# Kernel optimization log

Hardware: AMD Instinct MI355X
Metric: run time of the kernel (lower is better)

Reference implementation:

```python
import jax, jax.numpy as jnp
import numpy as np

B, N = 8192, 200  # batch of patches, fixed 200 points per patch


def setup_inputs() -> dict:
    key = jax.random.key(0)
    k1, = jax.random.split(key, 1)
    network_in = jax.random.normal(k1, (B, N, 13), dtype=jnp.float32)
    # learned parameters per build(): outward_shift init 0.25, a init 1, b init 0
    outward_shift = jnp.full((1,), 0.25, dtype=jnp.float32)
    a = jnp.ones((1,), dtype=jnp.float32)
    b = jnp.zeros((1,), dtype=jnp.float32)
    return {"network_in": network_in, "outward_shift": outward_shift, "a": a, "b": b}


def reference(network_in, outward_shift, a, b):
    w = network_in[:, :, 0:1]          # [B,N,1]
    xyz1 = network_in[:, :, 1:4]
    xyz2 = network_in[:, :, 4:7]       # also orig_xyz2
    norm1 = network_in[:, :, 7:10]
    norm2 = network_in[:, :, 10:13]

    w = jax.nn.relu(a * w + b) + 1e-8  # [B,N,1]

    v1 = xyz1 + norm1 * outward_shift
    v2 = xyz2 + norm2 * outward_shift

    w_sum = jnp.sum(w, axis=1)                       # [B,1]
    v1_ctr = jnp.sum(v1 * w, axis=1) / w_sum         # [B,3]
    v2_ctr = jnp.sum(v2 * w, axis=1) / w_sum         # [B,3]
    v1 = v1 - v1_ctr[:, None, :]
    v2 = v2 - v2_ctr[:, None, :]

    # cov = v2^T diag(w) v1, done without materializing the NxN diagonal
    cov = jnp.einsum('bni,bn,bnj->bij', v2, w[:, :, 0], v1)  # [B,3,3]

    # tf.linalg.svd: cov = u diag(s) v^T  ->  jnp svd: cov = u diag(s) vh, v = vh^T
    u, s, vh = jnp.linalg.svd(cov)
    v = jnp.swapaxes(vh, -1, -2)

    VUt = jnp.einsum('bik,bjk->bij', v, u)           # v @ u^T
    det_VUt = jnp.linalg.det(VUt)                    # [B]
    ones = jnp.ones_like(det_VUt)
    d = jnp.stack([ones, ones, det_VUt], axis=-1)    # [B,3]

    # R = v @ diag([1,1,det]) @ u^T
    R = jnp.einsum('bik,bk,bjk->bij', v, d, u)       # [B,3,3]

    t = v1_ctr - jnp.einsum('bij,bj->bi', R, v2_ctr) # [B,3]
    new_coords = jnp.einsum('bij,bnj->bni', R, xyz2) + t[:, None, :]
    return new_coords
```

## Files before the change

### kernel.cpp

```cpp
#include <hip/hip_runtime.h>
#include <math.h>

#define NPTS 200
#define NCH  13
#define BLK  256
#define FPB  (NPTS * NCH)

typedef float f4u __attribute__((ext_vector_type(4), aligned(4)));

__global__ __launch_bounds__(BLK) void reduce_kernel(
    const float* __restrict__ net_in,
    const float* __restrict__ shift_p,
    const float* __restrict__ a_p,
    const float* __restrict__ b_p,
    float* __restrict__ sums)
{
    __shared__ float s_in[4 * FPB];
    __shared__ float s_part[4][16][20];

    const int tid = threadIdx.x;
    const int w   = tid >> 6;
    const int l   = tid & 63;
    const int b   = blockIdx.x * 4 + w;

    const float shift = shift_p[0];
    const float aa    = a_p[0];
    const float bb    = b_p[0];

    const float* src = net_in + (size_t)b * FPB;
    float*       dst = s_in + w * FPB;

    #pragma unroll
    for (int j = 0; j < 10; ++j) {
        __builtin_amdgcn_global_load_lds(
            (const __attribute__((address_space(1))) void*)(src + j * 256 + l * 4),
            (__attribute__((address_space(3))) void*)(dst + j * 256),
            16, 0, 0);
    }
    if (l < 10) {
        __builtin_amdgcn_global_load_lds(
            (const __attribute__((address_space(1))) void*)(src + 2560 + l * 4),
            (__attribute__((address_space(3))) void*)(dst + 2560),
            16, 0, 0);
    }
    __builtin_amdgcn_s_waitcnt(0);
    __asm__ __volatile__("" ::: "memory");

    float acc[16];
    #pragma unroll
    for (int k = 0; k < 16; ++k) acc[k] = 0.f;

    #pragma unroll
    for (int j = 0; j < 4; ++j) {
        const int p = l + 64 * j;
        if (j < 3 || l < 8) {
            const float* q = dst + p * NCH;
            float wt = aa * q[0] + bb;
            wt = fmaxf(wt, 0.f) + 1e-8f;
            const float v1x = fmaf(shift, q[7],  q[1]);
            const float v1y = fmaf(shift, q[8],  q[2]);
            const float v1z = fmaf(shift, q[9],  q[3]);
            const float v2x = fmaf(shift, q[10], q[4]);
            const float v2y = fmaf(shift, q[11], q[5]);
            const float v2z = fmaf(shift, q[12], q[6]);
            const float wv2x = wt * v2x, wv2y = wt * v2y, wv2z = wt * v2z;
            acc[0] += wt;
            acc[1] += wt * v1x; acc[2] += wt * v1y; acc[3] += wt * v1z;
            acc[4] += wv2x;     acc[5] += wv2y;     acc[6] += wv2z;
            acc[7]  += wv2x * v1x; acc[8]  += wv2x * v1y; acc[9]  += wv2x * v1z;
            acc[10] += wv2y * v1x; acc[11] += wv2y * v1y; acc[12] += wv2y * v1z;
            acc[13] += wv2z * v1x; acc[14] += wv2z * v1y; acc[15] += wv2z * v1z;
        }
    }

    #pragma unroll
    for (int k = 0; k < 16; ++k) {
        acc[k] += __shfl_down(acc[k], 32, 64);
        acc[k] += __shfl_down(acc[k], 16, 64);
    }

    if (l < 16) {
        float4* pp = (float4*)&s_part[w][l][0];
        pp[0] = make_float4(acc[0],  acc[1],  acc[2],  acc[3]);
        pp[1] = make_float4(acc[4],  acc[5],  acc[6],  acc[7]);
        pp[2] = make_float4(acc[8],  acc[9],  acc[10], acc[11]);
        pp[3] = make_float4(acc[12], acc[13], acc[14], acc[15]);
    }
    if (l < 16) {
        float s = 0.f;
        #pragma unroll
        for (int r = 0; r < 16; ++r) s += s_part[w][r][l];
        sums[(size_t)b * 16 + l] = s;
    }
}

__global__ __launch_bounds__(BLK) void solve_kernel(
    const float* __restrict__ sums,
    float* __restrict__ Rt,
    int B)
{
    const int b = blockIdx.x * BLK + threadIdx.x;
    if (b >= B) return;

    float f[16];
    #pragma unroll
    for (int k = 0; k < 16; ++k) f[k] = sums[(size_t)b * 16 + k];

    const float W = f[0];
    const float invW = 1.0f / W;
    const float v1cx = f[1] * invW, v1cy = f[2] * invW, v1cz = f[3] * invW;
    const float v2cx = f[4] * invW, v2cy = f[5] * invW, v2cz = f[6] * invW;

    const float Sxx = f[7]  - W * v2cx * v1cx;
    const float Sxy = f[8]  - W * v2cx * v1cy;
    const float Sxz = f[9]  - W * v2cx * v1cz;
    const float Syx = f[10] - W * v2cy * v1cx;
    const float Syy = f[11] - W * v2cy * v1cy;
    const float Syz = f[12] - W * v2cy * v1cz;
    const float Szx = f[13] - W * v2cz * v1cx;
    const float Szy = f[14] - W * v2cz * v1cy;
    const float Szz = f[15] - W * v2cz * v1cz;

    float A[4][4];
    A[0][0] = Sxx + Syy + Szz;
    A[0][1] = Syz - Szy;  A[0][2] = Szx - Sxz;  A[0][3] = Sxy - Syx;
    A[1][1] = Sxx - Syy - Szz;
    A[1][2] = Sxy + Syx;  A[1][3] = Szx + Sxz;
    A[2][2] = -Sxx + Syy - Szz;
    A[2][3] = Syz + Szy;
    A[3][3] = -Sxx - Syy + Szz;
    A[1][0] = A[0][1]; A[2][0] = A[0][2]; A[3][0] = A[0][3];
    A[2][1] = A[1][2]; A[3][1] = A[1][3]; A[3][2] = A[2][3];

    float V[4][4] = {{1,0,0,0},{0,1,0,0},{0,0,1,0},{0,0,0,1}};

    const int prs[6][2] = {{0,1},{0,2},{0,3},{1,2},{1,3},{2,3}};
    for (int sweep = 0; sweep < 5; ++sweep) {
        #pragma unroll
        for (int r = 0; r < 6; ++r) {
            const int p = prs[r][0], q = prs[r][1];
            float apq = A[p][q];
            if (apq != 0.0f) {
                float tau = (A[q][q] - A[p][p]) / (2.0f * apq);
                float t = copysignf(1.0f, tau) /
                          (fabsf(tau) + sqrtf(1.0f + tau * tau));
                float c = rsqrtf(1.0f + t * t);
                float s = t * c;
                #pragma unroll
                for (int k = 0; k < 4; ++k) {
                    float a1 = A[p][k], a2 = A[q][k];
                    A[p][k] = c * a1 - s * a2;
                    A[q][k] = s * a1 + c * a2;
                }
                #pragma unroll
                for (int k = 0; k < 4; ++k) {
                    float a1 = A[k][p], a2 = A[k][q];
                    A[k][p] = c * a1 - s * a2;
                    A[k][q] = s * a1 + c * a2;
                }
                #pragma unroll
                for (int k = 0; k < 4; ++k) {
                    float a1 = V[k][p], a2 = V[k][q];
                    V[k][p] = c * a1 - s * a2;
                    V[k][q] = s * a1 + c * a2;
                }
            }
        }
    }

    int best = 0;
    #pragma unroll
    for (int i = 1; i < 4; ++i) if (A[i][i] > A[best][best]) best = i;
    const float q0 = V[0][best], qx = V[1][best], qy = V[2][best], qz = V[3][best];

    const float R00 = q0*q0 + qx*qx - qy*qy - qz*qz;
    const float R01 = 2.0f * (qx*qy - q0*qz);
    const float R02 = 2.0f * (qx*qz + q0*qy);
    const float R10 = 2.0f * (qx*qy + q0*qz);
    const float R11 = q0*q0 - qx*qx + qy*qy - qz*qz;
    const float R12 = 2.0f * (qy*qz - q0*qx);
    const float R20 = 2.0f * (qx*qz - q0*qy);
    const float R21 = 2.0f * (qy*qz + q0*qx);
    const float R22 = q0*q0 - qx*qx - qy*qy + qz*qz;

    float* o = Rt + (size_t)b * 12;
    o[0] = R00; o[1]  = R01; o[2]  = R02;
    o[3] = R10; o[4]  = R11; o[5]  = R12;
    o[6] = R20; o[7]  = R21; o[8]  = R22;
    o[9]  = v1cx - (R00 * v2cx + R01 * v2cy + R02 * v2cz);
    o[10] = v1cy - (R10 * v2cx + R11 * v2cy + R12 * v2cz);
    o[11] = v1cz - (R20 * v2cx + R21 * v2cy + R22 * v2cz);
}

__global__ __launch_bounds__(BLK) void apply_kernel(
    const float* __restrict__ net_in,
    const float* __restrict__ Rt,
    float* __restrict__ out,
    int total)
{
    const int g = blockIdx.x * BLK + threadIdx.x;
    if (g >= total) return;
    const int b = g / 50;
    const int q = g - b * 50;

    const float* r = Rt + (size_t)b * 12;
    const float R00 = r[0], R01 = r[1], R02 = r[2];
    const float R10 = r[3], R11 = r[4], R12 = r[5];
    const float R20 = r[6], R21 = r[7], R22 = r[8];
    const float t0  = r[9], t1  = r[10], t2 = r[11];

    const float* base = net_in + (size_t)b * FPB + (q * 4) * NCH;
    float nx[4], ny[4], nz[4];
    #pragma unroll
    for (int i = 0; i < 4; ++i) {
        const f4u v = *(const f4u*)(base + i * NCH + 4);
        nx[i] = R00 * v.x + R01 * v.y + R02 * v.z + t0;
        ny[i] = R10 * v.x + R11 * v.y + R12 * v.z + t1;
        nz[i] = R20 * v.x + R21 * v.y + R22 * v.z + t2;
    }

    float4* p = (float4*)(out + (size_t)b * (NPTS * 3)) + q * 3;
    p[0] = make_float4(nx[0], ny[0], nz[0], nx[1]);
    p[1] = make_float4(ny[1], nz[1], nx[2], ny[2]);
    p[2] = make_float4(nz[2], nx[3], ny[3], nz[3]);
}

extern "C" void kernel_launch(void* const* d_in, const int* in_sizes, int n_in,
                              void* d_out, int out_size, void* d_ws, size_t ws_size,
                              hipStream_t stream) {
    const float* net_in  = (const float*)d_in[0];
    const float* shift_p = (const float*)d_in[1];
    const float* a_p     = (const float*)d_in[2];
    const float* b_p     = (const float*)d_in[3];
    float* out = (float*)d_out;

    const int B = in_sizes[0] / FPB;

    float* sums = (float*)d_ws;
    float* Rt   = sums + (size_t)B * 16;

    reduce_kernel<<<B / 4, BLK, 0, stream>>>(net_in, shift_p, a_p, b_p, sums);
    solve_kernel<<<(B + BLK - 1) / BLK, BLK, 0, stream>>>(sums, Rt, B);
    apply_kernel<<<(B * 50 + BLK - 1) / BLK, BLK, 0, stream>>>(net_in, Rt, out, B * 50);
}
```

Baseline: 161.9 us.

## Fuse reduce, solve and apply into one wave-per-batch kernel

```diff
diff --git a/kernel.cpp b/kernel.cpp
--- a/kernel.cpp
+++ b/kernel.cpp
@@ -5,18 +5,39 @@
 #define NCH  13
 #define BLK  256
 #define FPB  (NPTS * NCH)
+#define STG  2560
 
 typedef float f4u __attribute__((ext_vector_type(4), aligned(4)));
 
-__global__ __launch_bounds__(BLK) void reduce_kernel(
+typedef struct { float x, y, z; } f3s;
+
+#define ACCUMULATE(Q0,Q1,Q2,Q3,Q4,Q5,Q6,Q7,Q8,Q9,Q10,Q11,Q12)               \
+    {                                                                        \
+        float wt = aa * (Q0) + bb;                                           \
+        wt = fmaxf(wt, 0.f) + 1e-8f;                                         \
+        const float v1x = fmaf(shift, (Q7),  (Q1));                          \
+        const float v1y = fmaf(shift, (Q8),  (Q2));                          \
+        const float v1z = fmaf(shift, (Q9),  (Q3));                          \
+        const float v2x = fmaf(shift, (Q10), (Q4));                          \
+        const float v2y = fmaf(shift, (Q11), (Q5));                          \
+        const float v2z = fmaf(shift, (Q12), (Q6));                          \
+        const float wv2x = wt * v2x, wv2y = wt * v2y, wv2z = wt * v2z;       \
+        acc[0] += wt;                                                        \
+        acc[1] += wt * v1x; acc[2] += wt * v1y; acc[3] += wt * v1z;          \
+        acc[4] += wv2x;     acc[5] += wv2y;     acc[6] += wv2z;              \
+        acc[7]  += wv2x * v1x; acc[8]  += wv2x * v1y; acc[9]  += wv2x * v1z; \
+        acc[10] += wv2y * v1x; acc[11] += wv2y * v1y; acc[12] += wv2y * v1z; \
+        acc[13] += wv2z * v1x; acc[14] += wv2z * v1y; acc[15] += wv2z * v1z; \
+    }
+
+__global__ __launch_bounds__(BLK, 4) void fused_kernel(
     const float* __restrict__ net_in,
     const float* __restrict__ shift_p,
     const float* __restrict__ a_p,
     const float* __restrict__ b_p,
-    float* __restrict__ sums)
+    float* __restrict__ out)
 {
-    __shared__ float s_in[4 * FPB];
-    __shared__ float s_part[4][16][20];
+    __shared__ float s_in[4 * STG];
 
     const int tid = threadIdx.x;
     const int w   = tid >> 6;
@@ -28,7 +49,7 @@
     const float bb    = b_p[0];
 
     const float* src = net_in + (size_t)b * FPB;
-    float*       dst = s_in + w * FPB;
+    float*       dst = s_in + w * STG;
 
     #pragma unroll
     for (int j = 0; j < 10; ++j) {
@@ -37,12 +58,19 @@
             (__attribute__((address_space(3))) void*)(dst + j * 256),
             16, 0, 0);
     }
-    if (l < 10) {
-        __builtin_amdgcn_global_load_lds(
-            (const __attribute__((address_space(1))) void*)(src + 2560 + l * 4),
-            (__attribute__((address_space(3))) void*)(dst + 2560),
-            16, 0, 0);
-    }
+
+    f4u t0v = {0.f, 0.f, 0.f, 0.f};
+    f4u t1v = {0.f, 0.f, 0.f, 0.f};
+    f4u t2v = {0.f, 0.f, 0.f, 0.f};
+    float t12 = 0.f;
+    if (l < 8) {
+        const float* tp = src + (192 + l) * NCH;
+        t0v = *(const f4u*)(tp);
+        t1v = *(const f4u*)(tp + 4);
+        t2v = *(const f4u*)(tp + 8);
+        t12 = tp[12];
+    }
+
     __builtin_amdgcn_s_waitcnt(0);
     __asm__ __volatile__("" ::: "memory");
 
@@ -50,128 +78,102 @@
     #pragma unroll
     for (int k = 0; k < 16; ++k) acc[k] = 0.f;
 
-    #pragma unroll
-    for (int j = 0; j < 4; ++j) {
+    float sx2[4], sy2[4], sz2[4];
+
+    #pragma unroll
+    for (int j = 0; j < 3; ++j) {
         const int p = l + 64 * j;
-        if (j < 3 || l < 8) {
-            const float* q = dst + p * NCH;
-            float wt = aa * q[0] + bb;
-            wt = fmaxf(wt, 0.f) + 1e-8f;
-            const float v1x = fmaf(shift, q[7],  q[1]);
-            const float v1y = fmaf(shift, q[8],  q[2]);
-            const float v1z = fmaf(shift, q[9],  q[3]);
-            const float v2x = fmaf(shift, q[10], q[4]);
-            const float v2y = fmaf(shift, q[11], q[5]);
-            const float v2z = fmaf(shift, q[12], q[6]);
-            const float wv2x = wt * v2x, wv2y = wt * v2y, wv2z = wt * v2z;
-            acc[0] += wt;
-            acc[1] += wt * v1x; acc[2] += wt * v1y; acc[3] += wt * v1z;
-            acc[4] += wv2x;     acc[5] += wv2y;     acc[6] += wv2z;
-            acc[7]  += wv2x * v1x; acc[8]  += wv2x * v1y; acc[9]  += wv2x * v1z;
-            acc[10] += wv2y * v1x; acc[11] += wv2y * v1y; acc[12] += wv2y * v1z;
-            acc[13] += wv2z * v1x; acc[14] += wv2z * v1y; acc[15] += wv2z * v1z;
-        }
+        const float* q = dst + p * NCH;
+        const float q0 = q[0],  q1 = q[1],  q2  = q[2],  q3  = q[3];
+        const float q4 = q[4],  q5 = q[5],  q6  = q[6],  q7  = q[7];
+        const float q8 = q[8],  q9 = q[9],  q10 = q[10], q11 = q[11], q12 = q[12];
+        ACCUMULATE(q0, q1, q2, q3, q4, q5, q6, q7, q8, q9, q10, q11, q12)
+        sx2[j] = q4; sy2[j] = q5; sz2[j] = q6;
+    }
+    sx2[3] = t1v.x; sy2[3] = t1v.y; sz2[3] = t1v.z;
+    if (l < 8) {
+        ACCUMULATE(t0v.x, t0v.y, t0v.z, t0v.w,
+                   t1v.x, t1v.y, t1v.z, t1v.w,
+                   t2v.x, t2v.y, t2v.z, t2v.w, t12)
     }
 
     #pragma unroll
     for (int k = 0; k < 16; ++k) {
-        acc[k] += __shfl_down(acc[k], 32, 64);
-        acc[k] += __shfl_down(acc[k], 16, 64);
-    }
-
-    if (l < 16) {
-        float4* pp = (float4*)&s_part[w][l][0];
-        pp[0] = make_float4(acc[0],  acc[1],  acc[2],  acc[3]);
-        pp[1] = make_float4(acc[4],  acc[5],  acc[6],  acc[7]);
-        pp[2] = make_float4(acc[8],  acc[9],  acc[10], acc[11]);
-        pp[3] = make_float4(acc[12], acc[13], acc[14], acc[15]);
-    }
-    if (l < 16) {
-        float s = 0.f;
-        #pragma unroll
-        for (int r = 0; r < 16; ++r) s += s_part[w][r][l];
-        sums[(size_t)b * 16 + l] = s;
-    }
-}
-
-__global__ __launch_bounds__(BLK) void solve_kernel(
-    const float* __restrict__ sums,
-    float* __restrict__ Rt,
-    int B)
-{
-    const int b = blockIdx.x * BLK + threadIdx.x;
-    if (b >= B) return;
-
-    float f[16];
-    #pragma unroll
-    for (int k = 0; k < 16; ++k) f[k] = sums[(size_t)b * 16 + k];
-
-    const float W = f[0];
+        acc[k] += __shfl_xor(acc[k], 32, 64);
+        acc[k] += __shfl_xor(acc[k], 16, 64);
+        acc[k] += __shfl_xor(acc[k],  8, 64);
+        acc[k] += __shfl_xor(acc[k],  4, 64);
+        acc[k] += __shfl_xor(acc[k],  2, 64);
+        acc[k] += __shfl_xor(acc[k],  1, 64);
+    }
+
+    const float W = acc[0];
     const float invW = 1.0f / W;
-    const float v1cx = f[1] * invW, v1cy = f[2] * invW, v1cz = f[3] * invW;
-    const float v2cx = f[4] * invW, v2cy = f[5] * invW, v2cz = f[6] * invW;
-
-    const float Sxx = f[7]  - W * v2cx * v1cx;
-    const float Sxy = f[8]  - W * v2cx * v1cy;
-    const float Sxz = f[9]  - W * v2cx * v1cz;
-    const float Syx = f[10] - W * v2cy * v1cx;
-    const float Syy = f[11] - W * v2cy * v1cy;
-    const float Syz = f[12] - W * v2cy * v1cz;
-    const float Szx = f[13] - W * v2cz * v1cx;
-    const float Szy = f[14] - W * v2cz * v1cy;
-    const float Szz = f[15] - W * v2cz * v1cz;
-
-    float A[4][4];
-    A[0][0] = Sxx + Syy + Szz;
-    A[0][1] = Syz - Szy;  A[0][2] = Szx - Sxz;  A[0][3] = Sxy - Syx;
-    A[1][1] = Sxx - Syy - Szz;
-    A[1][2] = Sxy + Syx;  A[1][3] = Szx + Sxz;
-    A[2][2] = -Sxx + Syy - Szz;
-    A[2][3] = Syz + Szy;
-    A[3][3] = -Sxx - Syy + Szz;
-    A[1][0] = A[0][1]; A[2][0] = A[0][2]; A[3][0] = A[0][3];
-    A[2][1] = A[1][2]; A[3][1] = A[1][3]; A[3][2] = A[2][3];
-
-    float V[4][4] = {{1,0,0,0},{0,1,0,0},{0,0,1,0},{0,0,0,1}};
+    const float v1cx = acc[1] * invW, v1cy = acc[2] * invW, v1cz = acc[3] * invW;
+    const float v2cx = acc[4] * invW, v2cy = acc[5] * invW, v2cz = acc[6] * invW;
+
+    const float Sxx = acc[7]  - W * v2cx * v1cx;
+    const float Sxy = acc[8]  - W * v2cx * v1cy;
+    const float Sxz = acc[9]  - W * v2cx * v1cz;
+    const float Syx = acc[10] - W * v2cy * v1cx;
+    const float Syy = acc[11] - W * v2cy * v1cy;
+    const float Syz = acc[12] - W * v2cy * v1cz;
+    const float Szx = acc[13] - W * v2cz * v1cx;
+    const float Szy = acc[14] - W * v2cz * v1cy;
+    const float Szz = acc[15] - W * v2cz * v1cz;
+
+    float Am[4][4];
+    Am[0][0] = Sxx + Syy + Szz;
+    Am[0][1] = Syz - Szy;  Am[0][2] = Szx - Sxz;  Am[0][3] = Sxy - Syx;
+    Am[1][1] = Sxx - Syy - Szz;
+    Am[1][2] = Sxy + Syx;  Am[1][3] = Szx + Sxz;
+    Am[2][2] = -Sxx + Syy - Szz;
+    Am[2][3] = Syz + Szy;
+    Am[3][3] = -Sxx - Syy + Szz;
+    Am[1][0] = Am[0][1]; Am[2][0] = Am[0][2]; Am[3][0] = Am[0][3];
+    Am[2][1] = Am[1][2]; Am[3][1] = Am[1][3]; Am[3][2] = Am[2][3];
+
+    float Vm[4][4] = {{1,0,0,0},{0,1,0,0},{0,0,1,0},{0,0,0,1}};
 
     const int prs[6][2] = {{0,1},{0,2},{0,3},{1,2},{1,3},{2,3}};
     for (int sweep = 0; sweep < 5; ++sweep) {
         #pragma unroll
         for (int r = 0; r < 6; ++r) {
             const int p = prs[r][0], q = prs[r][1];
-            float apq = A[p][q];
+            float apq = Am[p][q];
             if (apq != 0.0f) {
-                float tau = (A[q][q] - A[p][p]) / (2.0f * apq);
+                float tau = (Am[q][q] - Am[p][p]) / (2.0f * apq);
                 float t = copysignf(1.0f, tau) /
                           (fabsf(tau) + sqrtf(1.0f + tau * tau));
                 float c = rsqrtf(1.0f + t * t);
                 float s = t * c;
                 #pragma unroll
                 for (int k = 0; k < 4; ++k) {
-                    float a1 = A[p][k], a2 = A[q][k];
-                    A[p][k] = c * a1 - s * a2;
-                    A[q][k] = s * a1 + c * a2;
+                    float a1 = Am[p][k], a2 = Am[q][k];
+                    Am[p][k] = c * a1 - s * a2;
+                    Am[q][k] = s * a1 + c * a2;
                 }
                 #pragma unroll
                 for (int k = 0; k < 4; ++k) {
-                    float a1 = A[k][p], a2 = A[k][q];
-                    A[k][p] = c * a1 - s * a2;
-                    A[k][q] = s * a1 + c * a2;
+                    float a1 = Am[k][p], a2 = Am[k][q];
+                    Am[k][p] = c * a1 - s * a2;
+                    Am[k][q] = s * a1 + c * a2;
                 }
                 #pragma unroll
                 for (int k = 0; k < 4; ++k) {
-                    float a1 = V[k][p], a2 = V[k][q];
-                    V[k][p] = c * a1 - s * a2;
-                    V[k][q] = s * a1 + c * a2;
+                    float a1 = Vm[k][p], a2 = Vm[k][q];
+                    Vm[k][p] = c * a1 - s * a2;
+                    Vm[k][q] = s * a1 + c * a2;
                 }
             }
         }
     }
 
-    int best = 0;
-    #pragma unroll
-    for (int i = 1; i < 4; ++i) if (A[i][i] > A[best][best]) best = i;
-    const float q0 = V[0][best], qx = V[1][best], qy = V[2][best], qz = V[3][best];
+    float bd = Am[0][0];
+    float q0 = Vm[0][0], qx = Vm[1][0], qy = Vm[2][0], qz = Vm[3][0];
+    if (Am[1][1] > bd) { bd = Am[1][1]; q0 = Vm[0][1]; qx = Vm[1][1]; qy = Vm[2][1]; qz = Vm[3][1]; }
+    if (Am[2][2] > bd) { bd = Am[2][2]; q0 = Vm[0][2]; qx = Vm[1][2]; qy = Vm[2][2]; qz = Vm[3][2]; }
+    if (Am[3][3] > bd) { bd = Am[3][3]; q0 = Vm[0][3]; qx = Vm[1][3]; qy = Vm[2][3]; qz = Vm[3][3]; }
 
     const float R00 = q0*q0 + qx*qx - qy*qy - qz*qz;
     const float R01 = 2.0f * (qx*qy - q0*qz);
@@ -183,46 +185,23 @@
     const float R21 = 2.0f * (qy*qz + q0*qx);
     const float R22 = q0*q0 - qx*qx - qy*qy + qz*qz;
 
-    float* o = Rt + (size_t)b * 12;
-    o[0] = R00; o[1]  = R01; o[2]  = R02;
-    o[3] = R10; o[4]  = R11; o[5]  = R12;
-    o[6] = R20; o[7]  = R21; o[8]  = R22;
-    o[9]  = v1cx - (R00 * v2cx + R01 * v2cy + R02 * v2cz);
-    o[10] = v1cy - (R10 * v2cx + R11 * v2cy + R12 * v2cz);
-    o[11] = v1cz - (R20 * v2cx + R21 * v2cy + R22 * v2cz);
-}
-
-__global__ __launch_bounds__(BLK) void apply_kernel(
-    const float* __restrict__ net_in,
-    const float* __restrict__ Rt,
-    float* __restrict__ out,
-    int total)
-{
-    const int g = blockIdx.x * BLK + threadIdx.x;
-    if (g >= total) return;
-    const int b = g / 50;
-    const int q = g - b * 50;
-
-    const float* r = Rt + (size_t)b * 12;
-    const float R00 = r[0], R01 = r[1], R02 = r[2];
-    const float R10 = r[3], R11 = r[4], R12 = r[5];
-    const float R20 = r[6], R21 = r[7], R22 = r[8];
-    const float t0  = r[9], t1  = r[10], t2 = r[11];
-
-    const float* base = net_in + (size_t)b * FPB + (q * 4) * NCH;
-    float nx[4], ny[4], nz[4];
-    #pragma unroll
-    for (int i = 0; i < 4; ++i) {
-        const f4u v = *(const f4u*)(base + i * NCH + 4);
-        nx[i] = R00 * v.x + R01 * v.y + R02 * v.z + t0;
-        ny[i] = R10 * v.x + R11 * v.y + R12 * v.z + t1;
-        nz[i] = R20 * v.x + R21 * v.y + R22 * v.z + t2;
-    }
-
-    float4* p = (float4*)(out + (size_t)b * (NPTS * 3)) + q * 3;
-    p[0] = make_float4(nx[0], ny[0], nz[0], nx[1]);
-    p[1] = make_float4(ny[1], nz[1], nx[2], ny[2]);
-    p[2] = make_float4(nz[2], nx[3], ny[3], nz[3]);
+    const float tx = v1cx - (R00 * v2cx + R01 * v2cy + R02 * v2cz);
+    const float ty = v1cy - (R10 * v2cx + R11 * v2cy + R12 * v2cz);
+    const float tz = v1cz - (R20 * v2cx + R21 * v2cy + R22 * v2cz);
+
+    float* ob = out + (size_t)b * (NPTS * 3);
+    #pragma unroll
+    for (int j = 0; j < 4; ++j) {
+        if (j < 3 || l < 8) {
+            const int p = l + 64 * j;
+            const float X = sx2[j], Y = sy2[j], Z = sz2[j];
+            f3s o3;
+            o3.x = R00 * X + R01 * Y + R02 * Z + tx;
+            o3.y = R10 * X + R11 * Y + R12 * Z + ty;
+            o3.z = R20 * X + R21 * Y + R22 * Z + tz;
+            *(f3s*)(ob + p * 3) = o3;
+        }
+    }
 }
 
 extern "C" void kernel_launch(void* const* d_in, const int* in_sizes, int n_in,
@@ -235,11 +214,7 @@
     float* out = (float*)d_out;
 
     const int B = in_sizes[0] / FPB;
-
-    float* sums = (float*)d_ws;
-    float* Rt   = sums + (size_t)B * 16;
-
-    reduce_kernel<<<B / 4, BLK, 0, stream>>>(net_in, shift_p, a_p, b_p, sums);
-    solve_kernel<<<(B + BLK - 1) / BLK, BLK, 0, stream>>>(sums, Rt, B);
-    apply_kernel<<<(B * 50 + BLK - 1) / BLK, BLK, 0, stream>>>(net_in, Rt, out, B * 50);
+    (void)d_ws; (void)ws_size; (void)n_in; (void)out_size;
+
+    fused_kernel<<<B / 4, BLK, 0, stream>>>(net_in, shift_p, a_p, b_p, out);
 }
```

Result: no change. 162.5 us (+0.4%).
